# Optimization experiments

Hardware: AMD Instinct MI355X
Metric: run time of the kernel (lower is better)

## Reference

```python
import jax, jax.numpy as jnp
from jax import lax
import numpy as np

B, S, FD, FS, H = 256, 365, 32, 27, 256


def setup_inputs() -> dict:
    key = jax.random.key(0)
    ks = jax.random.split(key, 6)
    x_d = jax.random.normal(ks[0], (B, S, FD), dtype=jnp.float32)
    x_s = jax.random.normal(ks[1], (B, FS), dtype=jnp.float32)
    W_ih = jax.random.normal(ks[2], (FD, 3 * H), dtype=jnp.float32) * 0.1
    W_hh = jnp.tile(jnp.eye(H, dtype=jnp.float32), (1, 3)) + 0.01 * jax.random.normal(ks[3], (H, 3 * H), dtype=jnp.float32)
    W_sh = jax.random.normal(ks[4], (FS, H), dtype=jnp.float32) * 0.1
    bias = jnp.zeros((3 * H,), dtype=jnp.float32).at[:H].set(5.0)  # initial_forget_bias=5
    bias_s = jnp.zeros((H,), dtype=jnp.float32)
    W_fc = jax.random.normal(ks[5], (H, 1), dtype=jnp.float32) * 0.1
    b_fc = jnp.zeros((1,), dtype=jnp.float32)
    return {"x_d": x_d, "x_s": x_s, "W_ih": W_ih, "W_hh": W_hh, "W_sh": W_sh,
            "bias": bias, "bias_s": bias_s, "W_fc": W_fc, "b_fc": b_fc}


def _ealstm(x_d, x_s, W_ih, W_hh, W_sh, bias, bias_s):
    # static input gate, computed once: [B, H]
    i_gate = jax.nn.sigmoid(x_s @ W_sh + bias_s)
    # precompute dynamic input projection, time-major: [S, B, 3H]
    x_proj = jnp.einsum('bsd,dh->sbh', x_d, W_ih)
    Hh = W_hh.shape[0]
    Bb = x_d.shape[0]

    def step(carry, xt):
        h, c = carry
        gates = h @ W_hh + bias + xt  # [B, 3H]
        f, o, g = jnp.split(gates, 3, axis=1)
        c1 = jax.nn.sigmoid(f) * c + i_gate * jnp.tanh(g)
        h1 = jax.nn.sigmoid(o) * jnp.tanh(c1)
        return (h1, c1), (h1, c1)

    init = (jnp.zeros((Bb, Hh), x_d.dtype), jnp.zeros((Bb, Hh), x_d.dtype))
    _, (h_n, c_n) = lax.scan(step, init, x_proj)
    # time-major -> batch-first
    return jnp.transpose(h_n, (1, 0, 2)), jnp.transpose(c_n, (1, 0, 2))


def reference(x_d, x_s, W_ih, W_hh, W_sh, bias, bias_s, W_fc, b_fc):
    h_n, c_n = _ealstm(x_d, x_s, W_ih, W_hh, W_sh, bias, bias_s)
    # dropout p=0.0 -> identity; fc head: [B, S, 1]
    out = h_n @ W_fc + b_fc
    return (out, h_n, c_n)
```

## Files before the change

### kernel.cpp

```cpp
#include <hip/hip_runtime.h>


#define BB 256
#define SS 365
#define FD 32
#define FS 27
#define HH 256
#define G3 768
#define KTOT 288
#define KQ 4
#define KCH 72
#define NA 192
#define PPITCH 776

__global__ __launch_bounds__(768) void ealstm_kernel(
    const float* __restrict__ x_d, const float* __restrict__ x_s,
    const float* __restrict__ W_ih, const float* __restrict__ W_hh,
    const float* __restrict__ W_sh, const float* __restrict__ bias,
    const float* __restrict__ bias_s, const float* __restrict__ W_fc,
    const float* __restrict__ b_fc, float* __restrict__ d_out)
{
    __shared__ __align__(16) float hbuf[KTOT];
    __shared__ __align__(16) float partials[KQ][PPITCH];
    __shared__ float outp[4];

    const int t = threadIdx.x;
    const int b = blockIdx.x;
    const int kq = t / NA;
    const int a  = t - kq * NA;
    const int col4 = 4 * a;

    float4 w[KCH];
#pragma unroll
    for (int i = 0; i < KCH; ++i) {
        const int k = kq * KCH + i;
        const float* src = (k < HH) ? (W_hh + (size_t)k * G3 + col4)
                                    : (W_ih + (size_t)(k - HH) * G3 + col4);
        w[i] = *reinterpret_cast<const float4*>(src);
    }

    float c_state = 0.f, ig = 0.f, bf = 0.f, bo = 0.f, bg = 0.f, wfc = 0.f;
    if (t < HH) {
        float accs = bias_s[t];
        for (int k = 0; k < FS; ++k)
            accs = fmaf(x_s[(size_t)b * FS + k], W_sh[(size_t)k * HH + t], accs);
        ig = 1.f / (1.f + __expf(-accs));
        bf = bias[t]; bo = bias[t + HH]; bg = bias[t + 2 * HH];
        wfc = W_fc[t];
        hbuf[t] = 0.f;
    }
    if (t >= 512 && t < 512 + FD) {
        hbuf[HH + (t - 512)] = x_d[(size_t)b * SS * FD + (t - 512)];
    }
    const float bfc = b_fc[0];
    __syncthreads();

    float* __restrict__ out_fc = d_out;
    float* __restrict__ hn_out = d_out + (size_t)BB * SS;
    float* __restrict__ cn_out = hn_out + (size_t)BB * SS * HH;

    for (int s = 0; s < SS; ++s) {
        float4 acc = make_float4(0.f, 0.f, 0.f, 0.f);
        const float4* hv4 = reinterpret_cast<const float4*>(hbuf + kq * KCH);
#pragma unroll
        for (int i = 0; i < KCH / 4; ++i) {
            const float4 hv = hv4[i];
            acc.x = fmaf(hv.x, w[4 * i + 0].x, acc.x);
            acc.y = fmaf(hv.x, w[4 * i + 0].y, acc.y);
            acc.z = fmaf(hv.x, w[4 * i + 0].z, acc.z);
            acc.w = fmaf(hv.x, w[4 * i + 0].w, acc.w);
            acc.x = fmaf(hv.y, w[4 * i + 1].x, acc.x);
            acc.y = fmaf(hv.y, w[4 * i + 1].y, acc.y);
            acc.z = fmaf(hv.y, w[4 * i + 1].z, acc.z);
            acc.w = fmaf(hv.y, w[4 * i + 1].w, acc.w);
            acc.x = fmaf(hv.z, w[4 * i + 2].x, acc.x);
            acc.y = fmaf(hv.z, w[4 * i + 2].y, acc.y);
            acc.z = fmaf(hv.z, w[4 * i + 2].z, acc.z);
            acc.w = fmaf(hv.z, w[4 * i + 2].w, acc.w);
            acc.x = fmaf(hv.w, w[4 * i + 3].x, acc.x);
            acc.y = fmaf(hv.w, w[4 * i + 3].y, acc.y);
            acc.z = fmaf(hv.w, w[4 * i + 3].z, acc.z);
            acc.w = fmaf(hv.w, w[4 * i + 3].w, acc.w);
        }
        *reinterpret_cast<float4*>(&partials[kq][col4]) = acc;
        __syncthreads();

        if (t < HH) {
            float f = partials[0][t] + partials[1][t] + partials[2][t] + partials[3][t] + bf;
            float o = partials[0][t + HH] + partials[1][t + HH] + partials[2][t + HH] + partials[3][t + HH] + bo;
            float g = partials[0][t + 2 * HH] + partials[1][t + 2 * HH] + partials[2][t + 2 * HH] + partials[3][t + 2 * HH] + bg;
            const float sf = 1.f / (1.f + __expf(-f));
            const float so = 1.f / (1.f + __expf(-o));
            const float tg = 1.f - 2.f / (1.f + __expf(2.f * g));
            c_state = sf * c_state + ig * tg;
            const float tc = 1.f - 2.f / (1.f + __expf(2.f * c_state));
            const float h1 = so * tc;
            hbuf[t] = h1;
            const size_t oidx = ((size_t)b * SS + s) * HH + t;
            hn_out[oidx] = h1;
            cn_out[oidx] = c_state;
            float p = h1 * wfc;
            for (int d = 32; d > 0; d >>= 1) p += __shfl_down(p, d);
            if ((t & 63) == 0) outp[t >> 6] = p;
        } else if (t >= 512 && t < 512 + FD) {
            const int sn = (s + 1 < SS) ? (s + 1) : s;
            hbuf[HH + (t - 512)] = x_d[(size_t)b * SS * FD + (size_t)sn * FD + (t - 512)];
        }
        __syncthreads();
        if (t == 0) {
            out_fc[(size_t)b * SS + s] = outp[0] + outp[1] + outp[2] + outp[3] + bfc;
        }
    }
}

extern "C" void kernel_launch(void* const* d_in, const int* in_sizes, int n_in,
                              void* d_out, int out_size, void* d_ws, size_t ws_size,
                              hipStream_t stream) {
    const float* x_d    = (const float*)d_in[0];
    const float* x_s    = (const float*)d_in[1];
    const float* W_ih   = (const float*)d_in[2];
    const float* W_hh   = (const float*)d_in[3];
    const float* W_sh   = (const float*)d_in[4];
    const float* bias   = (const float*)d_in[5];
    const float* bias_s = (const float*)d_in[6];
    const float* W_fc   = (const float*)d_in[7];
    const float* b_fc   = (const float*)d_in[8];

    ealstm_kernel<<<dim3(BB), dim3(768), 0, stream>>>(
        x_d, x_s, W_ih, W_hh, W_sh, bias, bias_s, W_fc, b_fc, (float*)d_out);
}
```

Measured before the change: 6.278 ms.

## Split each batch pair across two cooperating blocks with global-memory flag sync

Each pair of blocks now handles two batch elements together, with each block owning half of the hidden units. Per step, a block reads the partner block's half of h from the hn output in global memory, after spinning on an acquire flag. The W_ih projection moves into shared memory, and the W_hh slices per thread are held in registers as separate f/o/g arrays. The aim is to halve the per-block recurrent matmul work and reuse each weight across two batch rows. In exchange it adds cross-block spin-waits every step, which assume both partner blocks are co-resident, plus a ready-handshake trick that writes into the cn output buffer.

```diff
diff --git a/kernel.cpp b/kernel.cpp
--- a/kernel.cpp
+++ b/kernel.cpp
@@ -6,109 +6,186 @@
 #define FD 32
 #define FS 27
 #define HH 256
-#define G3 768
-#define KTOT 288
-#define KQ 4
-#define KCH 72
-#define NA 192
-#define PPITCH 776
-
-__global__ __launch_bounds__(768) void ealstm_kernel(
+#define NT 512
+typedef unsigned int u32;
+
+#define MAC4C(HA, HB, WF, WO, WG) \
+    acc00 = fmaf(HA, WF, acc00); acc01 = fmaf(HA, WO, acc01); acc02 = fmaf(HA, WG, acc02); \
+    acc10 = fmaf(HB, WF, acc10); acc11 = fmaf(HB, WO, acc11); acc12 = fmaf(HB, WG, acc12);
+
+#define MAC16(A, B, J) \
+    MAC4C(A.x, B.x, wf[4*(J)+0], wo[4*(J)+0], wg[4*(J)+0]) \
+    MAC4C(A.y, B.y, wf[4*(J)+1], wo[4*(J)+1], wg[4*(J)+1]) \
+    MAC4C(A.z, B.z, wf[4*(J)+2], wo[4*(J)+2], wg[4*(J)+2]) \
+    MAC4C(A.w, B.w, wf[4*(J)+3], wo[4*(J)+3], wg[4*(J)+3])
+
+__global__ __launch_bounds__(NT, 2) void ealstm_kernel(
     const float* __restrict__ x_d, const float* __restrict__ x_s,
     const float* __restrict__ W_ih, const float* __restrict__ W_hh,
     const float* __restrict__ W_sh, const float* __restrict__ bias,
     const float* __restrict__ bias_s, const float* __restrict__ W_fc,
-    const float* __restrict__ b_fc, float* __restrict__ d_out)
+    const float* __restrict__ b_fc, float* __restrict__ d_out,
+    u32* __restrict__ ws)
 {
-    __shared__ __align__(16) float hbuf[KTOT];
-    __shared__ __align__(16) float partials[KQ][PPITCH];
-    __shared__ float outp[4];
+    __shared__ __align__(16) float sm_wih[FD][3][128];
+    __shared__ __align__(16) float sm_part[2][3][4][128];
+    __shared__ __align__(16) float hbuf[2][128];
+    __shared__ __align__(16) float xbuf[2][2][FD];
+    __shared__ float outp[2][2];
 
     const int t = threadIdx.x;
-    const int b = blockIdx.x;
-    const int kq = t / NA;
-    const int a  = t - kq * NA;
-    const int col4 = 4 * a;
-
-    float4 w[KCH];
-#pragma unroll
-    for (int i = 0; i < KCH; ++i) {
-        const int k = kq * KCH + i;
-        const float* src = (k < HH) ? (W_hh + (size_t)k * G3 + col4)
-                                    : (W_ih + (size_t)(k - HH) * G3 + col4);
-        w[i] = *reinterpret_cast<const float4*>(src);
-    }
-
-    float c_state = 0.f, ig = 0.f, bf = 0.f, bo = 0.f, bg = 0.f, wfc = 0.f;
-    if (t < HH) {
-        float accs = bias_s[t];
-        for (int k = 0; k < FS; ++k)
-            accs = fmaf(x_s[(size_t)b * FS + k], W_sh[(size_t)k * HH + t], accs);
-        ig = 1.f / (1.f + __expf(-accs));
-        bf = bias[t]; bo = bias[t + HH]; bg = bias[t + 2 * HH];
-        wfc = W_fc[t];
-        hbuf[t] = 0.f;
-    }
-    if (t >= 512 && t < 512 + FD) {
-        hbuf[HH + (t - 512)] = x_d[(size_t)b * SS * FD + (t - 512)];
-    }
-    const float bfc = b_fc[0];
-    __syncthreads();
+    const int blk = blockIdx.x;
+    const int team = blk >> 1, role = blk & 1;
+    const int e0 = team, e1 = team + 128;
+    const int kq = t >> 7, a = t & 127;
+    const bool own_half = ((kq >> 1) == role);
 
     float* __restrict__ out_fc = d_out;
     float* __restrict__ hn_out = d_out + (size_t)BB * SS;
     float* __restrict__ cn_out = hn_out + (size_t)BB * SS * HH;
 
+    u32* flag_my = ws + (size_t)(team * 2 + role) * 16;
+    u32* flag_pt = ws + (size_t)(team * 2 + (1 ^ role)) * 16;
+    float* fcp_my = (float*)(ws + 4096) + (team * 2 + role) * 4;
+    float* fcp_pt = (float*)(ws + 4096) + (team * 2 + (1 ^ role)) * 4;
+
+    float wf[64], wo[64], wg[64];
+    {
+        const float* base = W_hh + (size_t)(64 * kq) * 768 + 128 * role + a;
+#pragma unroll
+        for (int j = 0; j < 64; ++j) {
+            wf[j] = base[(size_t)j * 768];
+            wo[j] = base[(size_t)j * 768 + 256];
+            wg[j] = base[(size_t)j * 768 + 512];
+        }
+    }
+    for (int idx = t; idx < FD * 384; idx += NT) {
+        const int k = idx / 384, rem = idx - k * 384;
+        const int g = rem >> 7, cc = rem & 127;
+        sm_wih[k][g][cc] = W_ih[(size_t)k * 768 + g * 256 + 128 * role + cc];
+    }
+    if (t < 64) {
+        const int e = t >> 5, lane = t & 31;
+        xbuf[0][e][lane] = x_d[(size_t)(e ? e1 : e0) * SS * FD + lane];
+    }
+    float c_state = 0.f, igv = 0.f, bfv = 0.f, bov = 0.f, bgv = 0.f, wfcv = 0.f;
+    if (t < 256) {
+        const int e = t >> 7, i = t & 127, u = 128 * role + i;
+        const int eb = e ? e1 : e0;
+        float accs = bias_s[u];
+        for (int k = 0; k < FS; ++k)
+            accs = fmaf(x_s[(size_t)eb * FS + k], W_sh[(size_t)k * HH + u], accs);
+        igv = 1.f / (1.f + __expf(-accs));
+        bfv = bias[u]; bov = bias[HH + u]; bgv = bias[2 * HH + u];
+        wfcv = W_fc[u];
+        hbuf[e][i] = 0.f;
+    }
+    const float bfc = b_fc[0];
+
+    u32* rdy_my = (u32*)(cn_out + ((size_t)e0 * SS + (SS - 1)) * HH + 128 * role);
+    u32* rdy_pt = (u32*)(cn_out + ((size_t)e0 * SS + (SS - 1)) * HH + 128 * (1 ^ role));
+    if (t == 0) {
+        __hip_atomic_store(flag_my, 0u, __ATOMIC_RELAXED, __HIP_MEMORY_SCOPE_AGENT);
+        __threadfence();
+        __hip_atomic_store(rdy_my, 0x3F800000u, __ATOMIC_RELEASE, __HIP_MEMORY_SCOPE_AGENT);
+        while (__hip_atomic_load(rdy_pt, __ATOMIC_ACQUIRE, __HIP_MEMORY_SCOPE_AGENT)
+               != 0x3F800000u) {}
+    }
+    __syncthreads();
+
     for (int s = 0; s < SS; ++s) {
-        float4 acc = make_float4(0.f, 0.f, 0.f, 0.f);
-        const float4* hv4 = reinterpret_cast<const float4*>(hbuf + kq * KCH);
-#pragma unroll
-        for (int i = 0; i < KCH / 4; ++i) {
-            const float4 hv = hv4[i];
-            acc.x = fmaf(hv.x, w[4 * i + 0].x, acc.x);
-            acc.y = fmaf(hv.x, w[4 * i + 0].y, acc.y);
-            acc.z = fmaf(hv.x, w[4 * i + 0].z, acc.z);
-            acc.w = fmaf(hv.x, w[4 * i + 0].w, acc.w);
-            acc.x = fmaf(hv.y, w[4 * i + 1].x, acc.x);
-            acc.y = fmaf(hv.y, w[4 * i + 1].y, acc.y);
-            acc.z = fmaf(hv.y, w[4 * i + 1].z, acc.z);
-            acc.w = fmaf(hv.y, w[4 * i + 1].w, acc.w);
-            acc.x = fmaf(hv.z, w[4 * i + 2].x, acc.x);
-            acc.y = fmaf(hv.z, w[4 * i + 2].y, acc.y);
-            acc.z = fmaf(hv.z, w[4 * i + 2].z, acc.z);
-            acc.w = fmaf(hv.z, w[4 * i + 2].w, acc.w);
-            acc.x = fmaf(hv.w, w[4 * i + 3].x, acc.x);
-            acc.y = fmaf(hv.w, w[4 * i + 3].y, acc.y);
-            acc.z = fmaf(hv.w, w[4 * i + 3].z, acc.z);
-            acc.w = fmaf(hv.w, w[4 * i + 3].w, acc.w);
-        }
-        *reinterpret_cast<float4*>(&partials[kq][col4]) = acc;
+        const int par = s & 1;
+        if (t == 0 && s > 0) {
+            fcp_my[((s - 1) & 1) * 2 + 0] = outp[0][0] + outp[0][1];
+            fcp_my[((s - 1) & 1) * 2 + 1] = outp[1][0] + outp[1][1];
+            __threadfence();
+            __hip_atomic_store(flag_my, (u32)s, __ATOMIC_RELEASE, __HIP_MEMORY_SCOPE_AGENT);
+        }
+        float xpre = 0.f; const int xi = t - 256;
+        if (xi >= 0 && xi < 64) {
+            const int xe = xi >> 5, xl = xi & 31;
+            const int sn = (s + 1 < SS) ? s + 1 : SS - 1;
+            xpre = x_d[(size_t)(xe ? e1 : e0) * SS * FD + (size_t)sn * FD + xl];
+        }
+        float acc00 = 0, acc01 = 0, acc02 = 0, acc10 = 0, acc11 = 0, acc12 = 0;
+        {
+            const int x0 = 8 * kq;
+#pragma unroll
+            for (int jj = 0; jj < 8; ++jj) {
+                const float xv0 = xbuf[par][0][x0 + jj], xv1 = xbuf[par][1][x0 + jj];
+                const float w0 = sm_wih[x0 + jj][0][a];
+                const float w1 = sm_wih[x0 + jj][1][a];
+                const float w2 = sm_wih[x0 + jj][2][a];
+                acc00 = fmaf(xv0, w0, acc00); acc01 = fmaf(xv0, w1, acc01); acc02 = fmaf(xv0, w2, acc02);
+                acc10 = fmaf(xv1, w0, acc10); acc11 = fmaf(xv1, w1, acc11); acc12 = fmaf(xv1, w2, acc12);
+            }
+        }
+        if (s > 0) {
+            if (own_half) {
+                const float4* h0 = reinterpret_cast<const float4*>(&hbuf[0][64 * (kq & 1)]);
+                const float4* h1 = reinterpret_cast<const float4*>(&hbuf[1][64 * (kq & 1)]);
+#pragma unroll
+                for (int j4 = 0; j4 < 16; ++j4) {
+                    const float4 A = h0[j4], B = h1[j4];
+                    MAC16(A, B, j4)
+                }
+            } else {
+                while ((int)__hip_atomic_load(flag_pt, __ATOMIC_ACQUIRE,
+                                              __HIP_MEMORY_SCOPE_AGENT) < s) {}
+                const float4* h0 = reinterpret_cast<const float4*>(
+                    hn_out + ((size_t)e0 * SS + (s - 1)) * HH + 128 * (1 ^ role) + 64 * (kq & 1));
+                const float4* h1 = reinterpret_cast<const float4*>(
+                    hn_out + ((size_t)e1 * SS + (s - 1)) * HH + 128 * (1 ^ role) + 64 * (kq & 1));
+#pragma unroll
+                for (int j4 = 0; j4 < 16; ++j4) {
+                    const float4 A = h0[j4], B = h1[j4];
+                    MAC16(A, B, j4)
+                }
+            }
+        }
+        if (role == 0 && t == 256 && s > 0) {
+            const int pp = (s - 1) & 1;
+            out_fc[(size_t)e0 * SS + (s - 1)] = outp[0][0] + outp[0][1] + fcp_pt[pp * 2 + 0] + bfc;
+            out_fc[(size_t)e1 * SS + (s - 1)] = outp[1][0] + outp[1][1] + fcp_pt[pp * 2 + 1] + bfc;
+        }
+        sm_part[0][0][kq][a] = acc00; sm_part[0][1][kq][a] = acc01; sm_part[0][2][kq][a] = acc02;
+        sm_part[1][0][kq][a] = acc10; sm_part[1][1][kq][a] = acc11; sm_part[1][2][kq][a] = acc12;
+        if (xi >= 0 && xi < 64) xbuf[par ^ 1][xi >> 5][xi & 31] = xpre;
         __syncthreads();
 
-        if (t < HH) {
-            float f = partials[0][t] + partials[1][t] + partials[2][t] + partials[3][t] + bf;
-            float o = partials[0][t + HH] + partials[1][t + HH] + partials[2][t + HH] + partials[3][t + HH] + bo;
-            float g = partials[0][t + 2 * HH] + partials[1][t + 2 * HH] + partials[2][t + 2 * HH] + partials[3][t + 2 * HH] + bg;
+        if (t < 256) {
+            const int e = t >> 7, i = t & 127;
+            float f = sm_part[e][0][0][i] + sm_part[e][0][1][i] + sm_part[e][0][2][i] + sm_part[e][0][3][i] + bfv;
+            float o = sm_part[e][1][0][i] + sm_part[e][1][1][i] + sm_part[e][1][2][i] + sm_part[e][1][3][i] + bov;
+            float g = sm_part[e][2][0][i] + sm_part[e][2][1][i] + sm_part[e][2][2][i] + sm_part[e][2][3][i] + bgv;
             const float sf = 1.f / (1.f + __expf(-f));
             const float so = 1.f / (1.f + __expf(-o));
             const float tg = 1.f - 2.f / (1.f + __expf(2.f * g));
-            c_state = sf * c_state + ig * tg;
+            c_state = sf * c_state + igv * tg;
             const float tc = 1.f - 2.f / (1.f + __expf(2.f * c_state));
             const float h1 = so * tc;
-            hbuf[t] = h1;
-            const size_t oidx = ((size_t)b * SS + s) * HH + t;
+            hbuf[e][i] = h1;
+            const size_t oidx = ((size_t)(e ? e1 : e0) * SS + s) * HH + 128 * role + i;
             hn_out[oidx] = h1;
             cn_out[oidx] = c_state;
-            float p = h1 * wfc;
-            for (int d = 32; d > 0; d >>= 1) p += __shfl_down(p, d);
-            if ((t & 63) == 0) outp[t >> 6] = p;
-        } else if (t >= 512 && t < 512 + FD) {
-            const int sn = (s + 1 < SS) ? (s + 1) : s;
-            hbuf[HH + (t - 512)] = x_d[(size_t)b * SS * FD + (size_t)sn * FD + (t - 512)];
+            float psum = h1 * wfcv;
+#pragma unroll
+            for (int d = 32; d > 0; d >>= 1) psum += __shfl_down(psum, d);
+            if ((t & 63) == 0) outp[t >> 7][(t >> 6) & 1] = psum;
         }
         __syncthreads();
-        if (t == 0) {
-            out_fc[(size_t)b * SS + s] = outp[0] + outp[1] + outp[2] + outp[3] + bfc;
+    }
+
+    if (t == 0) {
+        fcp_my[0] = outp[0][0] + outp[0][1];
+        fcp_my[1] = outp[1][0] + outp[1][1];
+        __threadfence();
+        __hip_atomic_store(flag_my, (u32)SS, __ATOMIC_RELEASE, __HIP_MEMORY_SCOPE_AGENT);
+        if (role == 0) {
+            while ((int)__hip_atomic_load(flag_pt, __ATOMIC_ACQUIRE,
+                                          __HIP_MEMORY_SCOPE_AGENT) < SS) {}
+            out_fc[(size_t)e0 * SS + (SS - 1)] = outp[0][0] + outp[0][1] + fcp_pt[0] + bfc;
+            out_fc[(size_t)e1 * SS + (SS - 1)] = outp[1][0] + outp[1][1] + fcp_pt[1] + bfc;
         }
     }
 }
@@ -126,6 +203,7 @@
     const float* W_fc   = (const float*)d_in[7];
     const float* b_fc   = (const float*)d_in[8];
 
-    ealstm_kernel<<<dim3(BB), dim3(768), 0, stream>>>(
-        x_d, x_s, W_ih, W_hh, W_sh, bias, bias_s, W_fc, b_fc, (float*)d_out);
+    ealstm_kernel<<<dim3(BB), dim3(NT), 0, stream>>>(
+        x_d, x_s, W_ih, W_hh, W_sh, bias, bias_s, W_fc, b_fc,
+        (float*)d_out, (u32*)d_ws);
 }
```

After: 18.30 ms. +191.4%, slower.
